# Performance work log

Hardware: AMD Instinct MI355X
Metric: run time of the kernel (lower is better)

The kernel has to match this reference:

```python
import jax, jax.numpy as jnp
import numpy as np
import math

D_DT, D_STATE, D_CONV = 32, 16, 4
C, P, DM, DI = 16, 256, 512, 1024


def setup_inputs() -> dict:
    key = jax.random.key(0)
    ks = jax.random.split(key, 8)
    rn = lambda k, s, sc: jax.random.normal(k, s, jnp.float32) * sc
    # dt bias init as in the module
    u = jax.random.uniform(ks[6], (DI,), jnp.float32)
    dt_bias = jnp.clip(jnp.exp(u * (math.log(0.1) - math.log(0.001))), 0.001, None)
    inv_dt_bias = dt_bias + jnp.log(-jnp.expm1(-dt_bias))
    A_log = jnp.log(jnp.tile(jnp.arange(1, D_STATE + 1, dtype=jnp.float32)[None, :], (DI, 1)))
    return {
        "x": jax.random.normal(ks[0], (C, P, DM), jnp.float32),
        "ssm_state": jnp.zeros((C, DI, D_STATE), jnp.float32),
        "in_w": rn(ks[1], (2 * DI, DM), DM ** -0.5),
        "in_b": jnp.zeros((2 * DI,), jnp.float32),
        "conv_w": rn(ks[2], (DI, DI, D_CONV), (DI * D_CONV) ** -0.5),
        "conv_b": jnp.zeros((DI,), jnp.float32),
        "param_w": rn(ks[3], (D_DT + 2 * D_STATE, DI), DI ** -0.5),
        "param_b": jnp.zeros((D_DT + 2 * D_STATE,), jnp.float32),
        "dt_w": jax.random.uniform(ks[4], (DI, D_DT), jnp.float32, -D_DT ** -0.5, D_DT ** -0.5),
        "dt_b": inv_dt_bias,
        "out_w": rn(ks[5], (DM, DI), DI ** -0.5),
        "out_b": jnp.zeros((DM,), jnp.float32),
        "A_log": A_log,
        "D": jnp.ones((DI,), jnp.float32),
    }


def reference(x, ssm_state, in_w, in_b, conv_w, conv_b, param_w, param_b,
              dt_w, dt_b, out_w, out_b, A_log, D):
    # input projection -> x, z branches          [C,P,2*DI]
    xz = x @ in_w.T + in_b
    xi, z = jnp.split(xz, 2, axis=-1)            # each [C,P,DI]
    # 'same'-ish edge padding along patch axis, then full Conv1d (valid)
    pad = ((0, 0), (D_CONV // 2, (D_CONV + 1) // 2 - 1), (0, 0))
    xi = jnp.pad(xi, pad, mode='edge')
    xi = jnp.swapaxes(xi, -1, -2)                # [C,DI,P+D_CONV-1]
    xi = jax.lax.conv_general_dilated(xi, conv_w, (1,), 'VALID',
                                      dimension_numbers=('NCH', 'OIH', 'NCH'))
    xi = xi + conv_b[None, :, None]
    xi = jax.nn.gelu(jnp.swapaxes(xi, -1, -2))   # [C,P,DI]
    # selective params
    x_db = xi @ param_w.T + param_b              # [C,P,D_DT+2*D_STATE]
    dt, B, Cm = jnp.split(x_db, (D_DT, D_DT + D_STATE), axis=-1)
    dt = jax.nn.softplus(dt @ dt_w.T + dt_b)     # [C,P,DI]
    A = -jnp.exp(A_log)                          # [DI,D_STATE]
    dA = jnp.exp(jnp.einsum('cpd,dn->pcdn', dt, A))   # [P,C,DI,D_STATE]
    dB = jnp.einsum('cpd,cpn->pcdn', dt, B)            # [P,C,DI,D_STATE]
    z = jax.nn.gelu(z)                           # (gelu applied again inside step, as in source)
    Cm_t = jnp.swapaxes(Cm, 0, 1)                # [P,C,D_STATE]
    xi_t = jnp.swapaxes(xi, 0, 1)                # [P,C,DI]
    z_t = jnp.swapaxes(z, 0, 1)                  # [P,C,DI]

    def step(s, data):
        xt, zt, dAt, dBt, Ct = data
        s = s * dAt + xt[..., None] * dBt        # [C,DI,D_STATE]
        y = jnp.einsum('cdn,cn->cd', s, Ct) + D * xt
        return s, y * jax.nn.gelu(zt)            # double gelu: faithful to source

    ssm_state, y = jax.lax.scan(step, ssm_state, (xi_t, z_t, dA, dB, Cm_t))
    y = y @ out_w.T + out_b                      # [P,C,DM]
    return jnp.swapaxes(y, 0, 1), ssm_state
```

## Files before the change

kernel.cpp:

```cpp
#include <hip/hip_runtime.h>
#include <hip/hip_bf16.h>

typedef __hip_bfloat16 bf16;
typedef short bf16x8 __attribute__((ext_vector_type(8)));
typedef float f32x4 __attribute__((ext_vector_type(4)));

#define CC 16
#define PP 256
#define DMH 512
#define DIH 1024
#define MM (CC*PP)
#define NST 16
#define NDT 32
#define LOG2E 1.44269504088896f

__device__ __forceinline__ float b2f(bf16 v){ return __bfloat162float(v); }
__device__ __forceinline__ bf16  f2b(float v){ return __float2bfloat16(v); }

__device__ __forceinline__ float geluf(float x){
  const float u = x*(0.7978845608028654f + 0.035677408136300125f*x*x);
  const float e = __builtin_amdgcn_exp2f(2.885390081777927f*u);
  const float t = 1.0f - 2.0f*__builtin_amdgcn_rcpf(e + 1.0f);
  return 0.5f*x*(1.0f + t);
}
__device__ __forceinline__ float softplusf(float x){
  if (x > 20.0f) return x;
  const float e = __builtin_amdgcn_exp2f(x * LOG2E);
  return 0.6931471805599453f * __builtin_amdgcn_logf(1.0f + e);
}

__device__ __forceinline__ void g2l16(const bf16* g, bf16* l){
  __builtin_amdgcn_global_load_lds(
      (const __attribute__((address_space(1))) void*)g,
      (__attribute__((address_space(3))) void*)(uint32_t)(uintptr_t)l,
      16, 0, 0);
}

__global__ void prep_all(const float* __restrict__ x, const float* __restrict__ in_w,
                         const float* __restrict__ out_w, const float* __restrict__ param_w,
                         const float* __restrict__ conv_w, const float* __restrict__ dt_w,
                         const float* __restrict__ in_b, const float* __restrict__ conv_b,
                         float* __restrict__ cb2,
                         bf16* __restrict__ xbf, bf16* __restrict__ inwz,
                         bf16* __restrict__ outwb, bf16* __restrict__ pwb,
                         bf16* __restrict__ cwT, bf16* __restrict__ inwT,
                         bf16* __restrict__ dtwb)
{
  const int b = blockIdx.x, tid = threadIdx.x;
  if (b < 3136){
    const float* src; bf16* dst; int i;
    if (b < 2048)      { src = x;                       dst = xbf;   i = b*256 + tid; }
    else if (b < 2560) { src = in_w + (size_t)DIH*DMH;  dst = inwz;  i = (b-2048)*256 + tid; }
    else if (b < 3072) { src = out_w;                   dst = outwb; i = (b-2560)*256 + tid; }
    else               { src = param_w;                 dst = pwb;   i = (b-3072)*256 + tid; }
    float4 v = ((const float4*)src)[i];
    bf16 o[4] = {f2b(v.x), f2b(v.y), f2b(v.z), f2b(v.w)};
    *(ushort4*)&dst[(size_t)i*4] = *(const ushort4*)o;
  } else if (b < 7232){
    const size_t idx = (size_t)(b-3136)*256 + tid;
    const float4 v = *(const float4*)(conv_w + idx*4);
    cwT[idx]                     = f2b(v.x);
    cwT[(size_t)DIH*DIH   + idx] = f2b(v.y);
    cwT[(size_t)2*DIH*DIH + idx] = f2b(v.z);
    cwT[(size_t)3*DIH*DIH + idx] = f2b(v.w);
    __shared__ float ls[4];
    const int i = (int)(idx & 1023);
    float acc = (v.x + v.y + v.z + v.w) * in_b[i];
    for (int off = 32; off; off >>= 1) acc += __shfl_down(acc, off);
    if ((tid & 63) == 0) ls[tid >> 6] = acc;
    __syncthreads();
    if (tid == 0){
      const int o = (int)(idx >> 10);
      float tot = ls[0] + ls[1] + ls[2] + ls[3];
      if (((b - 3136) & 3) == 0) tot += conv_b[o];
      atomicAdd(&cb2[o], tot);
    }
  } else if (b < 7360){
    __shared__ float T[64][65];
    const int b2 = b - 7232;
    const int i0 = (b2 >> 3)*64, m0 = (b2 & 7)*64;
    const int r = tid >> 2, c0 = (tid & 3)*16;
    #pragma unroll
    for (int t = 0; t < 4; t++){
      float4 v = *(const float4*)&in_w[(size_t)(i0 + r)*DMH + m0 + c0 + t*4];
      T[r][c0+t*4+0] = v.x; T[r][c0+t*4+1] = v.y;
      T[r][c0+t*4+2] = v.z; T[r][c0+t*4+3] = v.w;
    }
    __syncthreads();
    bf16 o[16];
    #pragma unroll
    for (int t = 0; t < 16; t++) o[t] = f2b(T[c0 + t][r]);
    *(ushort4*)&inwT[(size_t)(m0 + r)*DIH + i0 + c0]      = *(const ushort4*)&o[0];
    *(ushort4*)&inwT[(size_t)(m0 + r)*DIH + i0 + c0 + 4]  = *(const ushort4*)&o[4];
    *(ushort4*)&inwT[(size_t)(m0 + r)*DIH + i0 + c0 + 8]  = *(const ushort4*)&o[8];
    *(ushort4*)&inwT[(size_t)(m0 + r)*DIH + i0 + c0 + 12] = *(const ushort4*)&o[12];
  } else {
    const int idx4 = (b-7360)*256 + tid;
    const int d = idx4 >> 4, k4 = (idx4 & 15)*4;
    bf16 o[4] = {};
    if (k4 < 32){
      const float4 v = *(const float4*)&dt_w[(size_t)d*NDT + k4];
      o[0]=f2b(v.x); o[1]=f2b(v.y); o[2]=f2b(v.z); o[3]=f2b(v.w);
    }
    *(ushort4*)&dtwb[(size_t)d*64 + k4] = *(const ushort4*)o;
  }
}

__global__ void reduce_cast(const float* __restrict__ pxz, const float* __restrict__ param_b,
                            float* __restrict__ bcg, bf16* __restrict__ xdbb){
  const int idx = blockIdx.x*256 + threadIdx.x;
  const int m = idx >> 4, k4 = (idx & 15)*4;
  float4 s = make_float4(0.f,0.f,0.f,0.f);
  #pragma unroll
  for (int z = 0; z < 8; z++){
    const float4 v = *(const float4*)&pxz[(size_t)z*MM*64 + (size_t)m*64 + k4];
    s.x += v.x; s.y += v.y; s.z += v.z; s.w += v.w;
  }
  const float4 pb = *(const float4*)&param_b[k4];
  s.x += pb.x; s.y += pb.y; s.z += pb.z; s.w += pb.w;
  if (k4 < 32){
    bf16 o[4] = {f2b(s.x), f2b(s.y), f2b(s.z), f2b(s.w)};
    *(ushort4*)&xdbb[(size_t)m*64 + k4] = *(const ushort4*)o;
  } else {
    bf16 o[4] = {};
    *(ushort4*)&xdbb[(size_t)m*64 + k4] = *(const ushort4*)o;
    *(float4*)&bcg[(size_t)m*32 + (k4 - 32)] = s;
  }
}

#define TBK 64

template<int EPI, int CONV, int NFRAG>
__launch_bounds__(256)
__global__ void mfma_gemm(const bf16* __restrict__ A, int lda,
                          const bf16* __restrict__ B, int ldb,
                          const float* __restrict__ bias,
                          float* __restrict__ outF,
                          bf16* __restrict__ outB0,
                          int ldo, int K, int azs, int ozs, int kzs)
{
  __shared__ bf16 As[128*TBK];
  __shared__ bf16 Bs[32*NFRAG*TBK];
  const int tid  = threadIdx.x;
  const int lane = tid & 63;
  const int wave = tid >> 6;
  const int wr = (wave >> 1) * 64;
  const int wc = (wave & 1) * 16 * NFRAG;
  const int mBase = blockIdx.x * 128;
  const int nBase = blockIdx.y * (32*NFRAG);
  A += (size_t)blockIdx.z * azs;
  const int nOff = blockIdx.z * ozs;
  const int koff = blockIdx.z * kzs;

  f32x4 acc[4][NFRAG] = {};

  for (int k0 = 0; k0 < K; k0 += TBK) {
    __syncthreads();
    #pragma unroll
    for (int it = 0; it < 4; it++) {
      const int idx = it*256 + tid;
      const int r = idx >> 3;
      const int cs = (idx & 7) ^ (r & 7);
      const bf16* ga;
      if (CONV) {
        const int tap = k0 >> 9, kk = k0 & 511;
        const int m = mBase + r;
        const int cc = m >> 8;
        int p = (m & 255) + tap - 2;
        p = min(max(p, 0), PP-1);
        ga = A + ((size_t)(cc*PP + p))*DMH + kk + cs*8;
      } else {
        ga = A + (size_t)(mBase + r)*lda + koff + k0 + cs*8;
      }
      g2l16(ga, &As[(size_t)idx*8]);
    }
    #pragma unroll
    for (int it = 0; it < NFRAG; it++) {
      const int idx = it*256 + tid;
      const int r = idx >> 3;
      const int cs = (idx & 7) ^ (r & 7);
      const bf16* gb = B + (size_t)(nBase + r)*ldb + koff + k0 + cs*8;
      g2l16(gb, &Bs[(size_t)idx*8]);
    }
    __syncthreads();
    #pragma unroll
    for (int ks = 0; ks < 2; ks++) {
      bf16x8 af[4], bfr[NFRAG];
      #pragma unroll
      for (int r = 0; r < 4; r++){
        const int rr = wr + r*16 + (lane & 15);
        const int ch = (ks*4 + (lane>>4)) ^ (rr & 7);
        af[r] = *(const bf16x8*)&As[rr*TBK + ch*8];
      }
      #pragma unroll
      for (int c = 0; c < NFRAG; c++){
        const int rn = wc + c*16 + (lane & 15);
        const int ch = (ks*4 + (lane>>4)) ^ (rn & 7);
        bfr[c] = *(const bf16x8*)&Bs[rn*TBK + ch*8];
      }
      #pragma unroll
      for (int r = 0; r < 4; r++)
        #pragma unroll
        for (int c = 0; c < NFRAG; c++)
          acc[r][c] = __builtin_amdgcn_mfma_f32_16x16x32_bf16(af[r], bfr[c], acc[r][c], 0, 0, 0);
    }
  }

  const int col0 = lane & 15;
  const int row0 = (lane >> 4) * 4;
  #pragma unroll
  for (int r = 0; r < 4; r++) {
    #pragma unroll
    for (int c = 0; c < NFRAG; c++) {
      #pragma unroll
      for (int reg = 0; reg < 4; reg++) {
        const int m = mBase + wr + r*16 + row0 + reg;
        const int n = nBase + wc + c*16 + col0;
        const float av = acc[r][c][reg];
        if (EPI == 0) {
          outF[(size_t)m*ldo + n] = av + bias[n];
        } else if (EPI == 1) {
          outB0[(size_t)m*ldo + n] = f2b(geluf(av + bias[n]));
        } else if (EPI == 2) {
          outB0[(size_t)m*ldo + n] = f2b(geluf(geluf(av + bias[n])));
        } else if (EPI == 3) {
          outB0[(size_t)m*ldo + n + nOff] = f2b(av);
        } else if (EPI == 5) {
          const float dtv = softplusf(av + bias[n]);
          const ushort ux = ((const ushort*)outF)[(size_t)m*DIH + n];
          bf16 xh; *(ushort*)&xh = ux;
          bf16 dA = f2b(dtv);
          bf16 dB = f2b(dtv * b2f(xh));
          const uint pk = (uint)(*(const ushort*)&dA) | ((uint)(*(const ushort*)&dB) << 16);
          ((uint*)outB0)[(size_t)m*ldo + n] = pk;
        } else if (EPI == 6) {
          outF[(size_t)m*ldo + n + nOff] = av;
        }
      }
    }
  }
}

__launch_bounds__(256, 2)
__global__ void scan_v5(const float* __restrict__ bcg, const bf16* __restrict__ xi,
                        const bf16* __restrict__ gz, const uint* __restrict__ pxg,
                        const float* __restrict__ A_log, const float* __restrict__ Dp,
                        const float* __restrict__ s0,
                        bf16* __restrict__ ypre, float* __restrict__ state_out)
{
  const int dg = blockIdx.x;
  const int tid = threadIdx.x;
  const int u = tid >> 7, ut = tid & 127;
  const int c = blockIdx.y*2 + u;
  const int dl = ut >> 3, ng = ut & 7;
  const int d0 = dg*16;
  const int d  = d0 + dl;
  const int base_m = c*PP;

  __shared__ float  bcT[2][3][16][36];
  __shared__ uint   pxT[2][3][16][20];
  __shared__ ushort xgT[2][3][16][40];
  __shared__ float  ybF[2][2][16][17];
  __shared__ ushort outT[2][16][24];
  __shared__ float  DvT[2][16];

  if (ut < 16) DvT[u][ut] = Dp[d0 + ut];
  const float2 al = *(const float2*)&A_log[(size_t)d*NST + 2*ng];
  const float a20 = -__expf(al.x)*LOG2E;
  const float a21 = -__expf(al.y)*LOG2E;
  float2 s = *(const float2*)&s0[((size_t)c*DIH + d)*NST + 2*ng];

  const int br = ut >> 3, bc4 = (ut & 7)*4;
  float4 bc_r; uint4 sec_r;

#define STAGE_LOAD(mm) do { \
    bc_r = *(const float4*)&bcg[(size_t)((mm) + br)*32 + bc4]; \
    if (ut < 64)      sec_r = *(const uint4*)&pxg[(size_t)((mm) + (ut>>2))*DIH + d0 + (ut&3)*4]; \
    else if (ut < 96) sec_r = *(const uint4*)&((const ushort*)xi)[(size_t)((mm) + ((ut-64)>>1))*DIH + d0 + ((ut-64)&1)*8]; \
    else              sec_r = *(const uint4*)&((const ushort*)gz)[(size_t)((mm) + ((ut-96)>>1))*DIH + d0 + ((ut-96)&1)*8]; \
  } while(0)
#define STAGE_COMMIT(nbuf) do { \
    *(float4*)&bcT[u][nbuf][br][bc4] = bc_r; \
    if (ut < 64)      *(uint4*)&pxT[u][nbuf][ut>>2][(ut&3)*4] = sec_r; \
    else if (ut < 96) *(uint4*)&xgT[u][nbuf][(ut-64)>>1][((ut-64)&1)*8] = sec_r; \
    else              *(uint4*)&xgT[u][nbuf][(ut-96)>>1][16 + ((ut-96)&1)*8] = sec_r; \
  } while(0)

  STAGE_LOAD(base_m);
  STAGE_COMMIT(0);
  __syncthreads();

  for (int g = 0; g < 16; ++g){
    const int buf = g % 3, nb = (g+1) % 3, yb = g & 1;
    const int m0 = base_m + g*16;
    if (g < 15) STAGE_LOAD(m0 + 16);
    float e0[16], e1[16], t0[16], t1[16], cx[16], cy[16];
    #pragma unroll
    for (int j = 0; j < 16; j++){
      const uint pk = pxT[u][buf][j][dl];
      const float2 Bv = *(const float2*)&bcT[u][buf][j][2*ng];
      const float2 Cv = *(const float2*)&bcT[u][buf][j][16 + 2*ng];
      const float dtv  = __int_as_float(pk << 16);
      const float dtxi = __int_as_float(pk & 0xffff0000u);
      e0[j] = __builtin_amdgcn_exp2f(dtv*a20);
      e1[j] = __builtin_amdgcn_exp2f(dtv*a21);
      t0[j] = dtxi*Bv.x; t1[j] = dtxi*Bv.y;
      cx[j] = Cv.x;      cy[j] = Cv.y;
    }
    #pragma unroll
    for (int j = 0; j < 16; j++){
      s.x = fmaf(s.x, e0[j], t0[j]);
      s.y = fmaf(s.y, e1[j], t1[j]);
      float y = fmaf(s.y, cy[j], s.x*cx[j]);
      int t;
      t = __builtin_amdgcn_update_dpp(0, __float_as_int(y), 0x111, 0xf, 0xf, true);
      y += __int_as_float(t);
      t = __builtin_amdgcn_update_dpp(0, __float_as_int(y), 0x112, 0xf, 0xf, true);
      y += __int_as_float(t);
      t = __builtin_amdgcn_update_dpp(0, __float_as_int(y), 0x114, 0xf, 0xf, true);
      y += __int_as_float(t);
      if (ng == 7) ybF[u][yb][j][dl] = y;
    }
    if (g < 15) STAGE_COMMIT(nb);
    __syncthreads();
    {
      const int ej = ut >> 3, eg = ut & 7;
      #pragma unroll
      for (int q = 0; q < 2; q++){
        const int ed = 2*eg + q;
        bf16 xh; *(ushort*)&xh = xgT[u][buf][ej][ed];
        bf16 gh; *(ushort*)&gh = xgT[u][buf][ej][16+ed];
        bf16 hv = f2b((ybF[u][yb][ej][ed] + DvT[u][ed]*b2f(xh)) * b2f(gh));
        outT[u][ej][ed] = *(const ushort*)&hv;
      }
      if (eg < 2)
        *(uint4*)((ushort*)ypre + (size_t)(m0+ej)*DIH + d0 + eg*8) = *(const uint4*)&outT[u][ej][eg*8];
    }
  }
  *(float2*)&state_out[((size_t)c*DIH + d)*NST + 2*ng] = s;
#undef STAGE_LOAD
#undef STAGE_COMMIT
}

extern "C" void kernel_launch(void* const* d_in, const int* in_sizes, int n_in,
                              void* d_out, int out_size, void* d_ws, size_t ws_size,
                              hipStream_t stream) {
  const float* x       = (const float*)d_in[0];
  const float* s0      = (const float*)d_in[1];
  const float* in_w    = (const float*)d_in[2];
  const float* in_b    = (const float*)d_in[3];
  const float* conv_w  = (const float*)d_in[4];
  const float* conv_b  = (const float*)d_in[5];
  const float* param_w = (const float*)d_in[6];
  const float* param_b = (const float*)d_in[7];
  const float* dt_w    = (const float*)d_in[8];
  const float* dt_b    = (const float*)d_in[9];
  const float* out_w   = (const float*)d_in[10];
  const float* out_b   = (const float*)d_in[11];
  const float* A_log   = (const float*)d_in[12];
  const float* Dp      = (const float*)d_in[13];

  char* ws = (char*)d_ws;
  bf16*   xi    = (bf16*)ws;   ws += (size_t)MM*DIH*2;
  bf16*   gz    = (bf16*)ws;   ws += (size_t)MM*DIH*2;
  float*  bcg   = (float*)ws;  ws += (size_t)MM*32*4;
  bf16*   xdbb  = (bf16*)ws;   ws += (size_t)MM*64*2;
  float*  cb2   = (float*)ws;  ws += 4096;
  bf16*   ypre  = (bf16*)ws;   ws += (size_t)MM*DIH*2;
  bf16*   outwb = (bf16*)ws;   ws += (size_t)DMH*DIH*2;
  bf16*   pwb   = (bf16*)ws;   ws += (size_t)64*DIH*2;
  bf16*   dtwb  = (bf16*)ws;   ws += (size_t)DIH*64*2;
  char*   U     = ws;          ws += (size_t)32*1024*1024;
  bf16* Wfb  = (bf16*)(U);
  bf16* xbf  = (bf16*)(U + (size_t) 4*1024*1024);
  bf16* inwz = (bf16*)(U + (size_t) 8*1024*1024);
  bf16* inwT = (bf16*)(U + (size_t) 9*1024*1024);
  bf16* cwT  = (bf16*)(U + (size_t)10*1024*1024);
  float* pxz = (float*)(U);
  uint*  pxg = (uint*)(U + (size_t)16*1024*1024);

  float* y_out  = (float*)d_out;
  float* st_out = y_out + (size_t)MM*DMH;

  hipMemsetAsync(cb2, 0, DIH*sizeof(float), stream);
  prep_all<<<7424, 256, 0, stream>>>(x, in_w, out_w, param_w, conv_w, dt_w,
                                     in_b, conv_b, cb2,
                                     xbf, inwz, outwb, pwb, cwT, inwT, dtwb);

  mfma_gemm<3,0,1><<<dim3(DIH/128, DMH/32, 4), 256, 0, stream>>>(
      cwT, DIH, inwT, DIH, nullptr, nullptr, Wfb, 4*DMH, DIH, DIH*DIH, DMH, 0);
  mfma_gemm<2,0,1><<<dim3(MM/128, DIH/32), 256, 0, stream>>>(
      xbf, DMH, inwz, DMH, in_b + DIH, nullptr, gz, DIH, DMH, 0, 0, 0);
  mfma_gemm<1,1,1><<<dim3(MM/128, DIH/32), 256, 0, stream>>>(
      xbf, DMH, Wfb, 4*DMH, cb2, nullptr, xi, DIH, 4*DMH, 0, 0, 0);
  mfma_gemm<6,0,1><<<dim3(MM/128, 2, 8), 256, 0, stream>>>(
      xi, DIH, pwb, DIH, nullptr, pxz, nullptr, 64, 128, 0, MM*64, 128);
  reduce_cast<<<256, 256, 0, stream>>>(pxz, param_b, bcg, xdbb);
  mfma_gemm<5,0,1><<<dim3(MM/128, DIH/32), 256, 0, stream>>>(
      xdbb, 64, dtwb, 64, dt_b, (float*)xi, (bf16*)pxg, DIH, 64, 0, 0, 0);
  scan_v5<<<dim3(64, CC/2), 256, 0, stream>>>(bcg, xi, gz, pxg, A_log, Dp,
                                              s0, ypre, st_out);
  mfma_gemm<0,0,1><<<dim3(MM/128, DMH/32), 256, 0, stream>>>(
      ypre, DIH, outwb, DIH, out_b, y_out, nullptr, DMH, DIH, 0, 0, 0);
}
```

Measured before the change: 224.6 us.

## Add dedicated conv GEMM sharing halo A tile across taps; slim dt handoff to scan

Replaces the generic CONV-mode GEMM (K=4*512, reloading A rows per tap) with a conv kernel that loads a 132-row halo tile of x once per k-chunk and reuses it for all four taps via shifted LDS reads, summing the per-tap accumulators in the epilogue. The dt GEMM epilogue now writes only bf16 softplus(dt) instead of a packed dt/dt*x pair, and the scan recomputes dt*x from xi it already loads. This removes the xi read in that epilogue and halves its output. The param projection split-K is reduced from 8 to 4 slices, so the reduce pass reads fewer partials. The conv kernel uses more LDS and more accumulator registers.

```diff
diff --git a/kernel.cpp b/kernel.cpp
--- a/kernel.cpp
+++ b/kernel.cpp
@@ -16,6 +16,7 @@
 
 __device__ __forceinline__ float b2f(bf16 v){ return __bfloat162float(v); }
 __device__ __forceinline__ bf16  f2b(float v){ return __float2bfloat16(v); }
+__device__ __forceinline__ float us2f(ushort u){ bf16 h; *(ushort*)&h = u; return __bfloat162float(h); }
 
 __device__ __forceinline__ float geluf(float x){
   const float u = x*(0.7978845608028654f + 0.035677408136300125f*x*x);
@@ -112,7 +113,7 @@
   const int m = idx >> 4, k4 = (idx & 15)*4;
   float4 s = make_float4(0.f,0.f,0.f,0.f);
   #pragma unroll
-  for (int z = 0; z < 8; z++){
+  for (int z = 0; z < 4; z++){
     const float4 v = *(const float4*)&pxz[(size_t)z*MM*64 + (size_t)m*64 + k4];
     s.x += v.x; s.y += v.y; s.z += v.z; s.w += v.w;
   }
@@ -130,7 +131,7 @@
 
 #define TBK 64
 
-template<int EPI, int CONV, int NFRAG>
+template<int EPI, int NFRAG>
 __launch_bounds__(256)
 __global__ void mfma_gemm(const bf16* __restrict__ A, int lda,
                           const bf16* __restrict__ B, int ldb,
@@ -161,17 +162,7 @@
       const int idx = it*256 + tid;
       const int r = idx >> 3;
       const int cs = (idx & 7) ^ (r & 7);
-      const bf16* ga;
-      if (CONV) {
-        const int tap = k0 >> 9, kk = k0 & 511;
-        const int m = mBase + r;
-        const int cc = m >> 8;
-        int p = (m & 255) + tap - 2;
-        p = min(max(p, 0), PP-1);
-        ga = A + ((size_t)(cc*PP + p))*DMH + kk + cs*8;
-      } else {
-        ga = A + (size_t)(mBase + r)*lda + koff + k0 + cs*8;
-      }
+      const bf16* ga = A + (size_t)(mBase + r)*lda + koff + k0 + cs*8;
       g2l16(ga, &As[(size_t)idx*8]);
     }
     #pragma unroll
@@ -219,20 +210,14 @@
         const float av = acc[r][c][reg];
         if (EPI == 0) {
           outF[(size_t)m*ldo + n] = av + bias[n];
-        } else if (EPI == 1) {
-          outB0[(size_t)m*ldo + n] = f2b(geluf(av + bias[n]));
         } else if (EPI == 2) {
           outB0[(size_t)m*ldo + n] = f2b(geluf(geluf(av + bias[n])));
         } else if (EPI == 3) {
           outB0[(size_t)m*ldo + n + nOff] = f2b(av);
         } else if (EPI == 5) {
           const float dtv = softplusf(av + bias[n]);
-          const ushort ux = ((const ushort*)outF)[(size_t)m*DIH + n];
-          bf16 xh; *(ushort*)&xh = ux;
-          bf16 dA = f2b(dtv);
-          bf16 dB = f2b(dtv * b2f(xh));
-          const uint pk = (uint)(*(const ushort*)&dA) | ((uint)(*(const ushort*)&dB) << 16);
-          ((uint*)outB0)[(size_t)m*ldo + n] = pk;
+          bf16 dh = f2b(dtv);
+          ((ushort*)outB0)[(size_t)m*ldo + n] = *(const ushort*)&dh;
         } else if (EPI == 6) {
           outF[(size_t)m*ldo + n + nOff] = av;
         }
@@ -241,9 +226,85 @@
   }
 }
 
+__launch_bounds__(256)
+__global__ void mfma_conv(const bf16* __restrict__ A,
+                          const bf16* __restrict__ B,
+                          const float* __restrict__ bias,
+                          bf16* __restrict__ outB)
+{
+  __shared__ bf16 As[132*64];
+  __shared__ bf16 Bs[128*64];
+  const int tid = threadIdx.x;
+  const int lane = tid & 63;
+  const int wave = tid >> 6;
+  const int wr = (wave >> 1) * 64;
+  const int wc = (wave & 1) * 16;
+  const int mBase = blockIdx.x * 128;
+  const int nBase = blockIdx.y * 32;
+  const int cc = mBase >> 8;
+  const int q  = mBase & 255;
+
+  f32x4 acc[4][4] = {};
+
+  for (int k0 = 0; k0 < DMH; k0 += 64) {
+    __syncthreads();
+    #pragma unroll
+    for (int it = 0; it < 5; it++) {
+      const int idx = it*256 + tid;
+      if (it < 4 || idx < 1056) {
+        const int h = idx >> 3;
+        const int cs = (idx & 7) ^ (h & 7);
+        int p = q - 2 + h;
+        p = min(max(p, 0), PP-1);
+        g2l16(A + ((size_t)(cc*PP + p))*DMH + k0 + cs*8, &As[(size_t)idx*8]);
+      }
+    }
+    #pragma unroll
+    for (int it = 0; it < 4; it++) {
+      const int idx = it*256 + tid;
+      const int r = idx >> 3;
+      const int tap = r >> 5, o = r & 31;
+      const int cs = (idx & 7) ^ (r & 7);
+      g2l16(B + (size_t)(nBase + o)*(4*DMH) + tap*DMH + k0 + cs*8, &Bs[(size_t)idx*8]);
+    }
+    __syncthreads();
+    #pragma unroll
+    for (int ks = 0; ks < 2; ks++) {
+      #pragma unroll
+      for (int t = 0; t < 4; t++) {
+        bf16x8 bft;
+        {
+          const int rn = t*32 + wc + (lane & 15);
+          const int ch = (ks*4 + (lane>>4)) ^ (rn & 7);
+          bft = *(const bf16x8*)&Bs[rn*64 + ch*8];
+        }
+        #pragma unroll
+        for (int r = 0; r < 4; r++) {
+          const int h = wr + r*16 + (lane & 15) + t;
+          const int ch = (ks*4 + (lane>>4)) ^ (h & 7);
+          bf16x8 af = *(const bf16x8*)&As[h*64 + ch*8];
+          acc[r][t] = __builtin_amdgcn_mfma_f32_16x16x32_bf16(af, bft, acc[r][t], 0, 0, 0);
+        }
+      }
+    }
+  }
+  const int col0 = lane & 15;
+  const int row0 = (lane >> 4) * 4;
+  #pragma unroll
+  for (int r = 0; r < 4; r++) {
+    #pragma unroll
+    for (int reg = 0; reg < 4; reg++) {
+      const int m = mBase + wr + r*16 + row0 + reg;
+      const int n = nBase + wc + col0;
+      const float av = acc[r][0][reg] + acc[r][1][reg] + acc[r][2][reg] + acc[r][3][reg];
+      outB[(size_t)m*DIH + n] = f2b(geluf(av + bias[n]));
+    }
+  }
+}
+
 __launch_bounds__(256, 2)
 __global__ void scan_v5(const float* __restrict__ bcg, const bf16* __restrict__ xi,
-                        const bf16* __restrict__ gz, const uint* __restrict__ pxg,
+                        const bf16* __restrict__ gz, const bf16* __restrict__ dtp,
                         const float* __restrict__ A_log, const float* __restrict__ Dp,
                         const float* __restrict__ s0,
                         bf16* __restrict__ ypre, float* __restrict__ state_out)
@@ -258,7 +319,7 @@
   const int base_m = c*PP;
 
   __shared__ float  bcT[2][3][16][36];
-  __shared__ uint   pxT[2][3][16][20];
+  __shared__ ushort dtT[2][3][16][24];
   __shared__ ushort xgT[2][3][16][40];
   __shared__ float  ybF[2][2][16][17];
   __shared__ ushort outT[2][16][24];
@@ -275,15 +336,15 @@
 
 #define STAGE_LOAD(mm) do { \
     bc_r = *(const float4*)&bcg[(size_t)((mm) + br)*32 + bc4]; \
-    if (ut < 64)      sec_r = *(const uint4*)&pxg[(size_t)((mm) + (ut>>2))*DIH + d0 + (ut&3)*4]; \
-    else if (ut < 96) sec_r = *(const uint4*)&((const ushort*)xi)[(size_t)((mm) + ((ut-64)>>1))*DIH + d0 + ((ut-64)&1)*8]; \
-    else              sec_r = *(const uint4*)&((const ushort*)gz)[(size_t)((mm) + ((ut-96)>>1))*DIH + d0 + ((ut-96)&1)*8]; \
+    if (ut < 32)      sec_r = *(const uint4*)&((const ushort*)dtp)[(size_t)((mm) + (ut>>1))*DIH + d0 + (ut&1)*8]; \
+    else if (ut < 64) sec_r = *(const uint4*)&((const ushort*)xi)[(size_t)((mm) + ((ut-32)>>1))*DIH + d0 + ((ut-32)&1)*8]; \
+    else if (ut < 96) sec_r = *(const uint4*)&((const ushort*)gz)[(size_t)((mm) + ((ut-64)>>1))*DIH + d0 + ((ut-64)&1)*8]; \
   } while(0)
 #define STAGE_COMMIT(nbuf) do { \
     *(float4*)&bcT[u][nbuf][br][bc4] = bc_r; \
-    if (ut < 64)      *(uint4*)&pxT[u][nbuf][ut>>2][(ut&3)*4] = sec_r; \
-    else if (ut < 96) *(uint4*)&xgT[u][nbuf][(ut-64)>>1][((ut-64)&1)*8] = sec_r; \
-    else              *(uint4*)&xgT[u][nbuf][(ut-96)>>1][16 + ((ut-96)&1)*8] = sec_r; \
+    if (ut < 32)      *(uint4*)&dtT[u][nbuf][ut>>1][(ut&1)*8] = sec_r; \
+    else if (ut < 64) *(uint4*)&xgT[u][nbuf][(ut-32)>>1][((ut-32)&1)*8] = sec_r; \
+    else if (ut < 96) *(uint4*)&xgT[u][nbuf][(ut-64)>>1][16 + ((ut-64)&1)*8] = sec_r; \
   } while(0)
 
   STAGE_LOAD(base_m);
@@ -297,11 +358,11 @@
     float e0[16], e1[16], t0[16], t1[16], cx[16], cy[16];
     #pragma unroll
     for (int j = 0; j < 16; j++){
-      const uint pk = pxT[u][buf][j][dl];
+      const float dtv = us2f(dtT[u][buf][j][dl]);
+      const float xiv = us2f(xgT[u][buf][j][dl]);
       const float2 Bv = *(const float2*)&bcT[u][buf][j][2*ng];
       const float2 Cv = *(const float2*)&bcT[u][buf][j][16 + 2*ng];
-      const float dtv  = __int_as_float(pk << 16);
-      const float dtxi = __int_as_float(pk & 0xffff0000u);
+      const float dtxi = dtv * xiv;
       e0[j] = __builtin_amdgcn_exp2f(dtv*a20);
       e1[j] = __builtin_amdgcn_exp2f(dtv*a21);
       t0[j] = dtxi*Bv.x; t1[j] = dtxi*Bv.y;
@@ -328,9 +389,8 @@
       #pragma unroll
       for (int q = 0; q < 2; q++){
         const int ed = 2*eg + q;
-        bf16 xh; *(ushort*)&xh = xgT[u][buf][ej][ed];
-        bf16 gh; *(ushort*)&gh = xgT[u][buf][ej][16+ed];
-        bf16 hv = f2b((ybF[u][yb][ej][ed] + DvT[u][ed]*b2f(xh)) * b2f(gh));
+        bf16 hv = f2b((ybF[u][yb][ej][ed] + DvT[u][ed]*us2f(xgT[u][buf][ej][ed]))
+                      * us2f(xgT[u][buf][ej][16+ed]));
         outT[u][ej][ed] = *(const ushort*)&hv;
       }
       if (eg < 2)
@@ -377,7 +437,7 @@
   bf16* inwT = (bf16*)(U + (size_t) 9*1024*1024);
   bf16* cwT  = (bf16*)(U + (size_t)10*1024*1024);
   float* pxz = (float*)(U);
-  uint*  pxg = (uint*)(U + (size_t)16*1024*1024);
+  bf16*  dtp = (bf16*)(U + (size_t)16*1024*1024);
 
   float* y_out  = (float*)d_out;
   float* st_out = y_out + (size_t)MM*DMH;
@@ -387,19 +447,18 @@
                                      in_b, conv_b, cb2,
                                      xbf, inwz, outwb, pwb, cwT, inwT, dtwb);
 
-  mfma_gemm<3,0,1><<<dim3(DIH/128, DMH/32, 4), 256, 0, stream>>>(
+  mfma_gemm<3,1><<<dim3(DIH/128, DMH/32, 4), 256, 0, stream>>>(
       cwT, DIH, inwT, DIH, nullptr, nullptr, Wfb, 4*DMH, DIH, DIH*DIH, DMH, 0);
-  mfma_gemm<2,0,1><<<dim3(MM/128, DIH/32), 256, 0, stream>>>(
+  mfma_gemm<2,1><<<dim3(MM/128, DIH/32), 256, 0, stream>>>(
       xbf, DMH, inwz, DMH, in_b + DIH, nullptr, gz, DIH, DMH, 0, 0, 0);
-  mfma_gemm<1,1,1><<<dim3(MM/128, DIH/32), 256, 0, stream>>>(
-      xbf, DMH, Wfb, 4*DMH, cb2, nullptr, xi, DIH, 4*DMH, 0, 0, 0);
-  mfma_gemm<6,0,1><<<dim3(MM/128, 2, 8), 256, 0, stream>>>(
-      xi, DIH, pwb, DIH, nullptr, pxz, nullptr, 64, 128, 0, MM*64, 128);
+  mfma_conv<<<dim3(MM/128, DIH/32), 256, 0, stream>>>(xbf, Wfb, cb2, xi);
+  mfma_gemm<6,1><<<dim3(MM/128, 2, 4), 256, 0, stream>>>(
+      xi, DIH, pwb, DIH, nullptr, pxz, nullptr, 64, 256, 0, MM*64, 256);
   reduce_cast<<<256, 256, 0, stream>>>(pxz, param_b, bcg, xdbb);
-  mfma_gemm<5,0,1><<<dim3(MM/128, DIH/32), 256, 0, stream>>>(
-      xdbb, 64, dtwb, 64, dt_b, (float*)xi, (bf16*)pxg, DIH, 64, 0, 0, 0);
-  scan_v5<<<dim3(64, CC/2), 256, 0, stream>>>(bcg, xi, gz, pxg, A_log, Dp,
+  mfma_gemm<5,1><<<dim3(MM/128, DIH/32), 256, 0, stream>>>(
+      xdbb, 64, dtwb, 64, dt_b, nullptr, (bf16*)dtp, DIH, 64, 0, 0, 0);
+  scan_v5<<<dim3(64, CC/2), 256, 0, stream>>>(bcg, xi, gz, dtp, A_log, Dp,
                                               s0, ypre, st_out);
-  mfma_gemm<0,0,1><<<dim3(MM/128, DMH/32), 256, 0, stream>>>(
+  mfma_gemm<0,1><<<dim3(MM/128, DMH/32), 256, 0, stream>>>(
       ypre, DIH, outwb, DIH, out_b, y_out, nullptr, DMH, DIH, 0, 0, 0);
 }
```

New measurement: 217.9 us. -3.0%, faster.
